# Optimization experiments

Hardware: AMD Instinct MI355X
Metric: run time of the kernel (lower is better)

Reference implementation:

```python
import jax, jax.numpy as jnp
import numpy as np
from jax import lax

FACTOR = 2
GAIN = 1.0
RESAMPLE = (1.0, 3.0, 3.0, 1.0)


def _setup_fir():
    k = np.asarray(RESAMPLE, dtype=np.float32)
    k = np.outer(k, k)
    k /= k.sum()
    return k * (GAIN * FACTOR ** 2)  # 4x4, scaled by factor^2 for upsampling


def setup_inputs() -> dict:
    key = jax.random.key(0)
    k1, k2, k3 = jax.random.split(key, 3)
    x = jax.random.normal(k1, (16, 256, 64, 64), jnp.float32)
    weight = jax.random.normal(k2, (256, 256, 3, 3), jnp.float32) * 0.05
    bias = jax.random.normal(k3, (256,), jnp.float32) * 0.05
    return {"x": x, "weight": weight, "bias": bias}


def _upsample_conv_2d(x, w):
    # Equivalent to torch: conv_transpose2d(x, flip(w).transpose(0,1), stride=FACTOR)
    # The pre-flip cancels conv_transpose's kernel flip, so this is an
    # input-dilated cross-correlation with the original OIHW weight.
    outC, inC, kh, kw = w.shape
    y = lax.conv_general_dilated(
        x, w, window_strides=(1, 1),
        padding=[(kh - 1, kh - 1), (kw - 1, kw - 1)],
        lhs_dilation=(FACTOR, FACTOR),
        dimension_numbers=('NCHW', 'OIHW', 'NCHW'))  # (N, outC, (H-1)*f+kh, (W-1)*f+kw)

    # upfirdn2d(y, fir, up=1, down=1, pad=((p+1)//2 + factor-1, p//2 + 1))
    fir = jnp.asarray(_setup_fir())
    fh, fw = fir.shape
    p = fh - FACTOR - (kw - 1)  # = 0 for k=3, factor=2, 4-tap FIR
    pad0 = (p + 1) // 2 + FACTOR - 1  # = 1
    pad1 = p // 2 + 1                  # = 1
    # upfirdn2d_native correlates with the flipped FIR, depthwise per channel
    dw = jnp.broadcast_to(fir[::-1, ::-1], (outC, 1, fh, fw))
    out = lax.conv_general_dilated(
        y, dw, window_strides=(1, 1),
        padding=[(pad0, pad1), (pad0, pad1)],
        feature_group_count=outC,
        dimension_numbers=('NCHW', 'OIHW', 'NCHW'))  # (N, outC, H*f, W*f)
    return out


def reference(x, weight, bias):
    out = _upsample_conv_2d(x, weight)
    return out + bias.reshape(1, -1, 1, 1)
```

## Files before the change

### kernel.cpp

```cpp
#include <hip/hip_runtime.h>
#include <hip/hip_bf16.h>

using bf16 = __hip_bfloat16;
typedef __bf16 bf16x8 __attribute__((ext_vector_type(8)));
typedef float f32x4 __attribute__((ext_vector_type(4)));
typedef short short8 __attribute__((ext_vector_type(8)));

#define AS1(p) ((const __attribute__((address_space(1))) void*)(p))
#define AS3(p) ((__attribute__((address_space(3))) void*)(p))

#define YSTRIDE 4368

__global__ void prep_wt_k(const float* __restrict__ w, bf16* __restrict__ wt) {
  const int o = blockIdx.x, i = threadIdx.x;
  const float* wp = w + (size_t)(o * 256 + i) * 9;
#pragma unroll
  for (int p = 0; p < 9; ++p)
    wt[(size_t)p * 65536 + o * 256 + i] = __float2bfloat16(wp[p]);
}

__global__ void zring_k(bf16* __restrict__ xpad) {
  const int bid = blockIdx.x;
  const int n = bid / 33, cg = bid - n * 33;
  const int t = threadIdx.x;
  const int cell = cg * 8 + (t >> 5);
  if (cell >= 260) return;
  int row, col;
  if (cell < 66) { row = 0; col = cell; }
  else if (cell < 132) { row = 65; col = cell - 66; }
  else if (cell < 196) { row = cell - 131; col = 0; }
  else { row = cell - 195; col = 65; }
  const int ch = (t & 31) * 8;
  short8 z = {0, 0, 0, 0, 0, 0, 0, 0};
  *(short8*)(xpad + (((size_t)n * 66 + row) * 66 + col) * 256 + ch) = z;
}

__global__ void xpose_k(const float* __restrict__ x, bf16* __restrict__ xpad) {
  const int b = blockIdx.x;
  const int icb = b & 3, iy = (b >> 2) & 63, n = b >> 8;
  __shared__ bf16 lds[64][72];
  const int t = threadIdx.x;
  const int c = t & 63, ixg = t >> 6;
  const float* src = x + (((size_t)(n * 256 + icb * 64 + c) * 64 + iy) * 64);
#pragma unroll
  for (int rep = 0; rep < 4; ++rep) {
    const int ix0 = ixg * 16 + rep * 4;
    float4 v = *reinterpret_cast<const float4*>(src + ix0);
    lds[ix0 + 0][c] = __float2bfloat16(v.x);
    lds[ix0 + 1][c] = __float2bfloat16(v.y);
    lds[ix0 + 2][c] = __float2bfloat16(v.z);
    lds[ix0 + 3][c] = __float2bfloat16(v.w);
  }
  __syncthreads();
  const int ix = t >> 2, cseg = (t & 3) * 16;
  bf16* dst = xpad + (((size_t)(n * 66 + iy + 1) * 66 + ix + 1) * 256 + icb * 64 + cseg);
  *reinterpret_cast<short8*>(dst) = *reinterpret_cast<const short8*>(&lds[ix][cseg]);
  *reinterpret_cast<short8*>(dst + 8) = *reinterpret_cast<const short8*>(&lds[ix][cseg + 8]);
}

__device__ __forceinline__ int xcdswz(int b, int n) {
  const int q = n >> 3, r = n & 7;
  const int xcd = b & 7, idx = b >> 3;
  return (xcd < r ? xcd * (q + 1) : r * (q + 1) + (xcd - r) * q) + idx;
}

template <int PLANE>
__device__ __forceinline__ void passA_body(int bid, const bf16* __restrict__ xpad,
                                           const bf16* __restrict__ wt,
                                           _Float16* __restrict__ yy, int nimg,
                                           bf16* ldsW, bf16* ldsX) {
  constexpr int M = (PLANE == 0) ? 4225 : (PLANE == 3) ? 4096 : 4160;
  constexpr int T = (M + 255) >> 8;
  constexpr int NT = (PLANE == 0) ? 4 : (PLANE == 3) ? 1 : 2;
  constexpr int AOFF = (PLANE >= 2) ? 1 : 0;
  constexpr int BOFF = (PLANE & 1) ? 1 : 0;
  constexpr int TAPI_all[4][4] = {{0, 2, 6, 8}, {1, 7, 0, 0}, {3, 5, 0, 0}, {4, 0, 0, 0}};
  constexpr int TDY_all[4][4] = {{0, 0, 1, 1}, {0, 1, 0, 0}, {0, 0, 0, 0}, {0, 0, 0, 0}};
  constexpr int TDX_all[4][4] = {{0, 1, 0, 1}, {0, 0, 0, 0}, {0, 1, 0, 0}, {0, 0, 0, 0}};

  const int t = threadIdx.x;
  const int oct = bid & 1;
  const int tmp = bid >> 1;
  const int tile = tmp % T;
  const int nl = tmp / T;
  const int m0 = tile * 256;
  const int oc0 = oct * 128;
  const bf16* xn = xpad + (size_t)nl * (66 * 66 * 256);
  _Float16* yn = yy + ((size_t)(PLANE * nimg + nl) * 256) * YSTRIDE;

  const int w = t >> 6, lane = t & 63;
  const int wr = w >> 2, wc = w & 3;
  const int lr = lane & 15, lg = lane >> 4;

  auto dec = [](int m, int& a, int& b) {
    if (PLANE == 0 || PLANE == 2) { a = m / 65; b = m - a * 65; }
    else { a = m >> 6; b = m & 63; }
  };

  int wOffB[2], xOffB[4];
#pragma unroll
  for (int r = 0; r < 2; ++r) {
    const int idx = r * 512 + t;
    const int row = idx >> 3;
    const int swz = ((idx & 7) * 16) ^ ((row & 7) << 4);
    wOffB[r] = ((oc0 + row) * 256) * 2 + swz;
  }
#pragma unroll
  for (int r = 0; r < 4; ++r) {
    const int idx = r * 512 + t;
    const int row = idx >> 3;
    const int swz = ((idx & 7) * 16) ^ ((row & 7) << 4);
    int m = m0 + row;
    if (m >= M) m = 0;
    int a, b;
    dec(m, a, b);
    xOffB[r] = (((a + AOFF) * 66 + (b + BOFF)) * 256) * 2 + swz;
  }

  f32x4 acc[4][4];
#pragma unroll
  for (int i = 0; i < 4; ++i)
#pragma unroll
    for (int j = 0; j < 4; ++j) acc[i][j] = (f32x4){0.f, 0.f, 0.f, 0.f};

  for (int ks = 0; ks < NT * 4; ++ks) {
    const int ti = ks >> 2, icb = ks & 3;
    const int xtoff = ((TDY_all[PLANE][ti] * 66 + TDX_all[PLANE][ti]) * 256 + icb * 64) * 2;
    const int wtoff = (TAPI_all[PLANE][ti] * 65536 + icb * 64) * 2;
#pragma unroll
    for (int r = 0; r < 2; ++r) {
      bf16* lw = ldsW + (size_t)(r * 512 + (t & 448)) * 8;
      __builtin_amdgcn_global_load_lds(AS1((const char*)wt + wOffB[r] + wtoff), AS3(lw), 16, 0, 0);
    }
#pragma unroll
    for (int r = 0; r < 4; ++r) {
      bf16* lx = ldsX + (size_t)(r * 512 + (t & 448)) * 8;
      __builtin_amdgcn_global_load_lds(AS1((const char*)xn + xOffB[r] + xtoff), AS3(lx), 16, 0, 0);
    }
    __syncthreads();

#pragma unroll
    for (int kk = 0; kk < 2; ++kk) {
      bf16x8 af[4], bfr[4];
#pragma unroll
      for (int i = 0; i < 4; ++i) {
        const int row = wr * 64 + i * 16 + lr;
        const int off = row * 128 + ((kk * 64 + lg * 16) ^ ((row & 7) << 4));
        af[i] = *(const bf16x8*)((const char*)ldsW + off);
      }
#pragma unroll
      for (int j = 0; j < 4; ++j) {
        const int row = wc * 64 + j * 16 + lr;
        const int off = row * 128 + ((kk * 64 + lg * 16) ^ ((row & 7) << 4));
        bfr[j] = *(const bf16x8*)((const char*)ldsX + off);
      }
#pragma unroll
      for (int i = 0; i < 4; ++i)
#pragma unroll
        for (int j = 0; j < 4; ++j)
          acc[i][j] = __builtin_amdgcn_mfma_f32_16x16x32_bf16(af[i], bfr[j], acc[i][j], 0, 0, 0);
    }
    __syncthreads();
  }

#pragma unroll
  for (int i = 0; i < 4; ++i) {
    const int ocb = oc0 + wr * 64 + i * 16 + lg * 4;
#pragma unroll
    for (int j = 0; j < 4; ++j) {
      const int m = m0 + wc * 64 + j * 16 + lr;
      if (m < M) {
        int a, b;
        dec(m, a, b);
        const size_t sp = (size_t)(a + 1) * 66 + (b + 1);
#pragma unroll
        for (int reg = 0; reg < 4; ++reg)
          yn[(size_t)(ocb + reg) * YSTRIDE + sp] = (_Float16)acc[i][j][reg];
      }
    }
  }
}

__global__ __launch_bounds__(512) void passA_all(const bf16* __restrict__ xpad,
                                                 const bf16* __restrict__ wt,
                                                 _Float16* __restrict__ yy, int nimg) {
  __shared__ __attribute__((aligned(16))) bf16 ldsW[128 * 64];
  __shared__ __attribute__((aligned(16))) bf16 ldsX[256 * 64];
  int bid = blockIdx.x;
  const int S0 = nimg * 34, S1 = nimg * 34, S2 = nimg * 34;
  if (bid < S0) { passA_body<0>(xcdswz(bid, S0), xpad, wt, yy, nimg, ldsW, ldsX); return; }
  bid -= S0;
  if (bid < S1) { passA_body<1>(xcdswz(bid, S1), xpad, wt, yy, nimg, ldsW, ldsX); return; }
  bid -= S1;
  if (bid < S2) { passA_body<2>(xcdswz(bid, S2), xpad, wt, yy, nimg, ldsW, ldsX); return; }
  bid -= S2;
  passA_body<3>(xcdswz(bid, nimg * 32), xpad, wt, yy, nimg, ldsW, ldsX);
}

__global__ void passB_k(const _Float16* __restrict__ yy, const float* __restrict__ bias,
                        float* __restrict__ out, int nimg, int n0) {
  __shared__ _Float16 ldsY[4][YSTRIDE];
  const int b = blockIdx.x;
  const int nl = b >> 8, c = b & 255;
  const int t = threadIdx.x;
  const size_t PS = (size_t)nimg * 256 * YSTRIDE;
  const _Float16* base = yy + ((size_t)nl * 256 + c) * YSTRIDE;

  for (int idx = t; idx < 4 * 546; idx += 256) {
    const int pl = idx / 546, off = idx - pl * 546;
    *(float4*)(&ldsY[pl][off * 8]) =
        *(const float4*)((const char*)(base + (size_t)pl * PS) + (size_t)off * 16);
  }
  __syncthreads();
  for (int idx = t; idx < 524; idx += 256) {
    if (idx < 132) {
      const int r = idx >> 1, col = (idx & 1) * 65;
      ldsY[1][r * 66 + col] = (_Float16)0.f;
    } else if (idx < 264) {
      const int e = idx - 132;
      const int row = (e >= 66) ? 65 : 0, col = (e >= 66) ? e - 66 : e;
      ldsY[2][row * 66 + col] = (_Float16)0.f;
    } else {
      const int e = idx - 264;
      int pos;
      if (e < 66) pos = e;
      else if (e < 132) pos = 65 * 66 + (e - 66);
      else if (e < 196) pos = (e - 131) * 66;
      else pos = (e - 195) * 66 + 65;
      ldsY[3][pos] = (_Float16)0.f;
    }
  }
  __syncthreads();

  const int p = t & 63, wv = t >> 6;
  const float bv = bias[c];
  float* ob = out + ((size_t)(n0 + nl) * 256 + c) * 16384;
  const int o0 = wv * 16;

  float eeA[2], eeB[2], oeA[2], oeB[2], oeC[2];
  float eoA[3], eoB[3], ooA[3], ooB[3], ooC[3];

#define LD2(dst, pl, row)                                  \
  { const int rb = (row) * 66 + p + 1;                     \
    dst[0] = (float)ldsY[pl][rb];                          \
    dst[1] = (float)ldsY[pl][rb + 1]; }
#define LD3(dst, pl, row)                                  \
  { const int rb = (row) * 66 + p;                         \
    dst[0] = (float)ldsY[pl][rb];                          \
    dst[1] = (float)ldsY[pl][rb + 1];                      \
    dst[2] = (float)ldsY[pl][rb + 2]; }

  LD2(eeA, 0, o0 + 1); LD2(eeB, 0, o0 + 2);
  LD2(oeA, 2, o0);     LD2(oeB, 2, o0 + 1); LD2(oeC, 2, o0 + 2);
  LD3(eoA, 1, o0 + 1); LD3(eoB, 1, o0 + 2);
  LD3(ooA, 3, o0);     LD3(ooB, 3, o0 + 1); LD3(ooC, 3, o0 + 2);

#pragma unroll
  for (int oi = 0; oi < 16; ++oi) {
    const int o = o0 + oi;
    float rce[2][2], rco[2][3];
#pragma unroll
    for (int cb = 0; cb < 2; ++cb) {
      rce[0][cb] = 0.75f * eeA[cb] + 0.25f * eeB[cb] + 0.25f * oeA[cb] + 0.75f * oeB[cb];
      rce[1][cb] = 0.25f * eeA[cb] + 0.75f * eeB[cb] + 0.75f * oeB[cb] + 0.25f * oeC[cb];
    }
#pragma unroll
    for (int cf = 0; cf < 3; ++cf) {
      rco[0][cf] = 0.75f * eoA[cf] + 0.25f * eoB[cf] + 0.25f * ooA[cf] + 0.75f * ooB[cf];
      rco[1][cf] = 0.25f * eoA[cf] + 0.75f * eoB[cf] + 0.75f * ooB[cf] + 0.25f * ooC[cf];
    }
#pragma unroll
    for (int py = 0; py < 2; ++py) {
      const float v0 = 0.75f * rce[py][0] + 0.25f * rce[py][1] + 0.25f * rco[py][0] +
                       0.75f * rco[py][1] + bv;
      const float v1 = 0.25f * rce[py][0] + 0.75f * rce[py][1] + 0.75f * rco[py][1] +
                       0.25f * rco[py][2] + bv;
      float2 st = {v0, v1};
      *(float2*)(ob + ((size_t)(2 * o + py)) * 128 + 2 * p) = st;
    }
    if (oi < 15) {
#pragma unroll
      for (int cb = 0; cb < 2; ++cb) {
        eeA[cb] = eeB[cb]; oeA[cb] = oeB[cb]; oeB[cb] = oeC[cb];
      }
#pragma unroll
      for (int cf = 0; cf < 3; ++cf) {
        eoA[cf] = eoB[cf]; ooA[cf] = ooB[cf]; ooB[cf] = ooC[cf];
      }
      LD2(eeB, 0, o + 3);
      LD2(oeC, 2, o + 3);
      LD3(eoB, 1, o + 3);
      LD3(ooC, 3, o + 3);
    }
  }
#undef LD2
#undef LD3
}

extern "C" void kernel_launch(void* const* d_in, const int* in_sizes, int n_in,
                              void* d_out, int out_size, void* d_ws, size_t ws_size,
                              hipStream_t stream) {
  const float* x = (const float*)d_in[0];
  const float* wgt = (const float*)d_in[1];
  const float* bias = (const float*)d_in[2];
  float* out = (float*)d_out;

  const size_t XPL = (size_t)66 * 66 * 256;
  const size_t YPN = (size_t)4 * 256 * YSTRIDE;
  const size_t WT_BYTES = (size_t)9 * 256 * 256 * 2;
  int c = 0;
  const int cands[5] = {16, 8, 4, 2, 1};
  for (int ci = 0; ci < 5; ++ci)
    if (WT_BYTES + (size_t)cands[ci] * (XPL + YPN) * 2 <= ws_size) { c = cands[ci]; break; }
  if (c == 0) return;

  bf16* wt = (bf16*)d_ws;
  bf16* xpad = (bf16*)((char*)d_ws + WT_BYTES);
  _Float16* yy = (_Float16*)((char*)d_ws + WT_BYTES + (size_t)c * XPL * 2);

  prep_wt_k<<<256, 256, 0, stream>>>(wgt, wt);

  for (int k = 0; k < 16 / c; ++k) {
    zring_k<<<c * 33, 256, 0, stream>>>(xpad);
    xpose_k<<<c * 256, 256, 0, stream>>>(x + (size_t)k * c * 1048576, xpad);
    passA_all<<<c * 134, 512, 0, stream>>>(xpad, wt, yy, c);
    passB_k<<<c * 256, 256, 0, stream>>>(yy, bias, out, c, k * c);
  }
}
```

Measured before the change: 287.8 us.

## Widen GEMM tile to all 256 output channels and split FIR pass by row halves

The polyphase GEMM pass now has each block compute all 256 output channels for a 256-pixel tile instead of 128. Each wave holds a 64x128 accumulator, so the x tile is loaded once per block rather than twice and grid size is halved. This raises register pressure (128 accumulator floats per lane) and doubles LDS for weights, which may reduce occupancy. Separately, the FIR/bias pass splits each channel plane into two 32-row halves, doubling block count and halving LDS per block to improve parallelism.

Result: faster. 273.7 us (-4.9%).

```diff
diff --git a/kernel.cpp b/kernel.cpp
--- a/kernel.cpp
+++ b/kernel.cpp
@@ -79,17 +79,14 @@
   constexpr int TDX_all[4][4] = {{0, 1, 0, 1}, {0, 0, 0, 0}, {0, 1, 0, 0}, {0, 0, 0, 0}};
 
   const int t = threadIdx.x;
-  const int oct = bid & 1;
-  const int tmp = bid >> 1;
-  const int tile = tmp % T;
-  const int nl = tmp / T;
+  const int tile = bid % T;
+  const int nl = bid / T;
   const int m0 = tile * 256;
-  const int oc0 = oct * 128;
   const bf16* xn = xpad + (size_t)nl * (66 * 66 * 256);
   _Float16* yn = yy + ((size_t)(PLANE * nimg + nl) * 256) * YSTRIDE;
 
   const int w = t >> 6, lane = t & 63;
-  const int wr = w >> 2, wc = w & 3;
+  const int wr = w >> 1, wc = w & 1;
   const int lr = lane & 15, lg = lane >> 4;
 
   auto dec = [](int m, int& a, int& b) {
@@ -97,19 +94,13 @@
     else { a = m >> 6; b = m & 63; }
   };
 
-  int wOffB[2], xOffB[4];
-#pragma unroll
-  for (int r = 0; r < 2; ++r) {
-    const int idx = r * 512 + t;
-    const int row = idx >> 3;
-    const int swz = ((idx & 7) * 16) ^ ((row & 7) << 4);
-    wOffB[r] = ((oc0 + row) * 256) * 2 + swz;
-  }
+  int wOffB[4], xOffB[4];
 #pragma unroll
   for (int r = 0; r < 4; ++r) {
     const int idx = r * 512 + t;
     const int row = idx >> 3;
     const int swz = ((idx & 7) * 16) ^ ((row & 7) << 4);
+    wOffB[r] = (row * 256) * 2 + swz;
     int m = m0 + row;
     if (m >= M) m = 0;
     int a, b;
@@ -117,18 +108,18 @@
     xOffB[r] = (((a + AOFF) * 66 + (b + BOFF)) * 256) * 2 + swz;
   }
 
-  f32x4 acc[4][4];
+  f32x4 acc[4][8];
 #pragma unroll
   for (int i = 0; i < 4; ++i)
 #pragma unroll
-    for (int j = 0; j < 4; ++j) acc[i][j] = (f32x4){0.f, 0.f, 0.f, 0.f};
+    for (int j = 0; j < 8; ++j) acc[i][j] = (f32x4){0.f, 0.f, 0.f, 0.f};
 
   for (int ks = 0; ks < NT * 4; ++ks) {
     const int ti = ks >> 2, icb = ks & 3;
     const int xtoff = ((TDY_all[PLANE][ti] * 66 + TDX_all[PLANE][ti]) * 256 + icb * 64) * 2;
     const int wtoff = (TAPI_all[PLANE][ti] * 65536 + icb * 64) * 2;
 #pragma unroll
-    for (int r = 0; r < 2; ++r) {
+    for (int r = 0; r < 4; ++r) {
       bf16* lw = ldsW + (size_t)(r * 512 + (t & 448)) * 8;
       __builtin_amdgcn_global_load_lds(AS1((const char*)wt + wOffB[r] + wtoff), AS3(lw), 16, 0, 0);
     }
@@ -141,7 +132,7 @@
 
 #pragma unroll
     for (int kk = 0; kk < 2; ++kk) {
-      bf16x8 af[4], bfr[4];
+      bf16x8 af[4], bfr[8];
 #pragma unroll
       for (int i = 0; i < 4; ++i) {
         const int row = wr * 64 + i * 16 + lr;
@@ -149,15 +140,15 @@
         af[i] = *(const bf16x8*)((const char*)ldsW + off);
       }
 #pragma unroll
-      for (int j = 0; j < 4; ++j) {
-        const int row = wc * 64 + j * 16 + lr;
+      for (int j = 0; j < 8; ++j) {
+        const int row = wc * 128 + j * 16 + lr;
         const int off = row * 128 + ((kk * 64 + lg * 16) ^ ((row & 7) << 4));
         bfr[j] = *(const bf16x8*)((const char*)ldsX + off);
       }
 #pragma unroll
       for (int i = 0; i < 4; ++i)
 #pragma unroll
-        for (int j = 0; j < 4; ++j)
+        for (int j = 0; j < 8; ++j)
           acc[i][j] = __builtin_amdgcn_mfma_f32_16x16x32_bf16(af[i], bfr[j], acc[i][j], 0, 0, 0);
     }
     __syncthreads();
@@ -165,10 +156,10 @@
 
 #pragma unroll
   for (int i = 0; i < 4; ++i) {
-    const int ocb = oc0 + wr * 64 + i * 16 + lg * 4;
-#pragma unroll
-    for (int j = 0; j < 4; ++j) {
-      const int m = m0 + wc * 64 + j * 16 + lr;
+    const int ocb = wr * 64 + i * 16 + lg * 4;
+#pragma unroll
+    for (int j = 0; j < 8; ++j) {
+      const int m = m0 + wc * 128 + j * 16 + lr;
       if (m < M) {
         int a, b;
         dec(m, a, b);
@@ -184,50 +175,50 @@
 __global__ __launch_bounds__(512) void passA_all(const bf16* __restrict__ xpad,
                                                  const bf16* __restrict__ wt,
                                                  _Float16* __restrict__ yy, int nimg) {
-  __shared__ __attribute__((aligned(16))) bf16 ldsW[128 * 64];
+  __shared__ __attribute__((aligned(16))) bf16 ldsW[256 * 64];
   __shared__ __attribute__((aligned(16))) bf16 ldsX[256 * 64];
   int bid = blockIdx.x;
-  const int S0 = nimg * 34, S1 = nimg * 34, S2 = nimg * 34;
+  const int S0 = nimg * 17, S1 = nimg * 17, S2 = nimg * 17;
   if (bid < S0) { passA_body<0>(xcdswz(bid, S0), xpad, wt, yy, nimg, ldsW, ldsX); return; }
   bid -= S0;
   if (bid < S1) { passA_body<1>(xcdswz(bid, S1), xpad, wt, yy, nimg, ldsW, ldsX); return; }
   bid -= S1;
   if (bid < S2) { passA_body<2>(xcdswz(bid, S2), xpad, wt, yy, nimg, ldsW, ldsX); return; }
   bid -= S2;
-  passA_body<3>(xcdswz(bid, nimg * 32), xpad, wt, yy, nimg, ldsW, ldsX);
-}
+  passA_body<3>(xcdswz(bid, nimg * 16), xpad, wt, yy, nimg, ldsW, ldsX);
+}
+
+#define BSTRIDE 2248
 
 __global__ void passB_k(const _Float16* __restrict__ yy, const float* __restrict__ bias,
                         float* __restrict__ out, int nimg, int n0) {
-  __shared__ _Float16 ldsY[4][YSTRIDE];
+  __shared__ _Float16 ldsY[4][BSTRIDE];
   const int b = blockIdx.x;
-  const int nl = b >> 8, c = b & 255;
+  const int h = b & 1, c = (b >> 1) & 255, nl = b >> 9;
+  const int R0 = h * 32;
   const int t = threadIdx.x;
   const size_t PS = (size_t)nimg * 256 * YSTRIDE;
   const _Float16* base = yy + ((size_t)nl * 256 + c) * YSTRIDE;
 
-  for (int idx = t; idx < 4 * 546; idx += 256) {
-    const int pl = idx / 546, off = idx - pl * 546;
+  for (int idx = t; idx < 4 * 281; idx += 256) {
+    const int pl = idx / 281, off = idx - pl * 281;
     *(float4*)(&ldsY[pl][off * 8]) =
-        *(const float4*)((const char*)(base + (size_t)pl * PS) + (size_t)off * 16);
+        *(const float4*)((const char*)(base + (size_t)pl * PS) + R0 * 132 + (size_t)off * 16);
   }
   __syncthreads();
-  for (int idx = t; idx < 524; idx += 256) {
-    if (idx < 132) {
+  const int brel = h ? 33 : 0;
+  for (int idx = t; idx < 268; idx += 256) {
+    if (idx < 68) {
       const int r = idx >> 1, col = (idx & 1) * 65;
       ldsY[1][r * 66 + col] = (_Float16)0.f;
-    } else if (idx < 264) {
-      const int e = idx - 132;
-      const int row = (e >= 66) ? 65 : 0, col = (e >= 66) ? e - 66 : e;
-      ldsY[2][row * 66 + col] = (_Float16)0.f;
+    } else if (idx < 134) {
+      ldsY[2][brel * 66 + (idx - 68)] = (_Float16)0.f;
+    } else if (idx < 200) {
+      ldsY[3][brel * 66 + (idx - 134)] = (_Float16)0.f;
     } else {
-      const int e = idx - 264;
-      int pos;
-      if (e < 66) pos = e;
-      else if (e < 132) pos = 65 * 66 + (e - 66);
-      else if (e < 196) pos = (e - 131) * 66;
-      else pos = (e - 195) * 66 + 65;
-      ldsY[3][pos] = (_Float16)0.f;
+      const int k = idx - 200;
+      const int r = k >> 1, col = (k & 1) * 65;
+      ldsY[3][r * 66 + col] = (_Float16)0.f;
     }
   }
   __syncthreads();
@@ -235,7 +226,7 @@
   const int p = t & 63, wv = t >> 6;
   const float bv = bias[c];
   float* ob = out + ((size_t)(n0 + nl) * 256 + c) * 16384;
-  const int o0 = wv * 16;
+  const int r0 = wv * 8;
 
   float eeA[2], eeB[2], oeA[2], oeB[2], oeC[2];
   float eoA[3], eoB[3], ooA[3], ooB[3], ooC[3];
@@ -250,14 +241,14 @@
     dst[1] = (float)ldsY[pl][rb + 1];                      \
     dst[2] = (float)ldsY[pl][rb + 2]; }
 
-  LD2(eeA, 0, o0 + 1); LD2(eeB, 0, o0 + 2);
-  LD2(oeA, 2, o0);     LD2(oeB, 2, o0 + 1); LD2(oeC, 2, o0 + 2);
-  LD3(eoA, 1, o0 + 1); LD3(eoB, 1, o0 + 2);
-  LD3(ooA, 3, o0);     LD3(ooB, 3, o0 + 1); LD3(ooC, 3, o0 + 2);
-
-#pragma unroll
-  for (int oi = 0; oi < 16; ++oi) {
-    const int o = o0 + oi;
+  LD2(eeA, 0, r0 + 1); LD2(eeB, 0, r0 + 2);
+  LD2(oeA, 2, r0);     LD2(oeB, 2, r0 + 1); LD2(oeC, 2, r0 + 2);
+  LD3(eoA, 1, r0 + 1); LD3(eoB, 1, r0 + 2);
+  LD3(ooA, 3, r0);     LD3(ooB, 3, r0 + 1); LD3(ooC, 3, r0 + 2);
+
+#pragma unroll
+  for (int oi = 0; oi < 8; ++oi) {
+    const int o = R0 + r0 + oi;
     float rce[2][2], rco[2][3];
 #pragma unroll
     for (int cb = 0; cb < 2; ++cb) {
@@ -278,7 +269,7 @@
       float2 st = {v0, v1};
       *(float2*)(ob + ((size_t)(2 * o + py)) * 128 + 2 * p) = st;
     }
-    if (oi < 15) {
+    if (oi < 7) {
 #pragma unroll
       for (int cb = 0; cb < 2; ++cb) {
         eeA[cb] = eeB[cb]; oeA[cb] = oeB[cb]; oeB[cb] = oeC[cb];
@@ -287,10 +278,10 @@
       for (int cf = 0; cf < 3; ++cf) {
         eoA[cf] = eoB[cf]; ooA[cf] = ooB[cf]; ooB[cf] = ooC[cf];
       }
-      LD2(eeB, 0, o + 3);
-      LD2(oeC, 2, o + 3);
-      LD3(eoB, 1, o + 3);
-      LD3(ooC, 3, o + 3);
+      LD2(eeB, 0, r0 + oi + 3);
+      LD2(oeC, 2, r0 + oi + 3);
+      LD3(eoB, 1, r0 + oi + 3);
+      LD3(ooC, 3, r0 + oi + 3);
     }
   }
 #undef LD2
@@ -323,7 +314,7 @@
   for (int k = 0; k < 16 / c; ++k) {
     zring_k<<<c * 33, 256, 0, stream>>>(xpad);
     xpose_k<<<c * 256, 256, 0, stream>>>(x + (size_t)k * c * 1048576, xpad);
-    passA_all<<<c * 134, 512, 0, stream>>>(xpad, wt, yy, c);
-    passB_k<<<c * 256, 256, 0, stream>>>(yy, bias, out, c, k * c);
-  }
-}
+    passA_all<<<c * 67, 512, 0, stream>>>(xpad, wt, yy, c);
+    passB_k<<<c * 512, 256, 0, stream>>>(yy, bias, out, c, k * c);
+  }
+}
```
